# Optimization experiments

Hardware: AMD Instinct MI355X
Metric: run time of the kernel (lower is better)

The kernel has to match this reference:

```python
import jax, jax.numpy as jnp
import numpy as np

B, S, E, H = 2, 2048, 1024, 16
D = E // H  # head_dim = 64


def setup_inputs() -> dict:
    key = jax.random.key(0)
    ks = jax.random.split(key, 4)
    return {
        "hidden_states": jax.random.normal(ks[0], (B, S, E), jnp.float32),
        "qk_weight": jax.random.normal(ks[1], (E, 2 * E), jnp.float32) * 0.02,
        "qk_bias": jnp.zeros((2 * E,), jnp.float32),
        "v_weight": jax.random.normal(ks[2], (E, E), jnp.float32) * 0.02,
        "v_resid_gain": jnp.ones((), jnp.float32),
        "v_skip_gain": jnp.ones((), jnp.float32),
        "proj_weight": jax.random.normal(ks[3], (E, E), jnp.float32) * 0.02,
        "proj_resid_gain": jnp.ones((), jnp.float32),
        "proj_skip_gain": jnp.ones((), jnp.float32),
        "attn_mat_resid_gain": jnp.ones((H,), jnp.float32),
        "attn_mat_skip_gain": jnp.ones((H,), jnp.float32),
        "centre_attn_gain": jnp.ones((H,), jnp.float32),
    }


def reference(hidden_states, qk_weight, qk_bias, v_weight, v_resid_gain,
              v_skip_gain, proj_weight, proj_resid_gain, proj_skip_gain,
              attn_mat_resid_gain, attn_mat_skip_gain, centre_attn_gain):
    b, s, e = hidden_states.shape
    dt = hidden_states.dtype
    eye_e = jnp.eye(e, dtype=dt)

    # qk_attn: MyConv1D (standard linear), split into query/key
    qk = hidden_states @ qk_weight + qk_bias
    q, k = jnp.split(qk, 2, axis=-1)
    # v_attn: skip MyConv1D -> x @ (resid_gain * W + skip_gain * I), no bias
    v = hidden_states @ (v_resid_gain * v_weight + v_skip_gain * eye_e)

    def split_heads(t):  # [b,s,e] -> [b,h,s,d]
        return t.reshape(b, s, H, D).transpose(0, 2, 1, 3)

    q, k, v = split_heads(q), split_heads(k), split_heads(v)

    # scaled causal attention scores
    scores = jnp.einsum('bhqd,bhkd->bhqk', q, k) / jnp.asarray(D, dt) ** 0.5
    causal = jnp.tril(jnp.ones((s, s), bool))
    scores = jnp.where(causal, scores, jnp.finfo(dt).min)
    attn = jax.nn.softmax(scores, axis=-1)

    # shaped attention: gain-mix softmax probs with identity and causal-uniform
    uniform = jnp.tril(jnp.ones((s, s), dt) / jnp.arange(1, s + 1, dtype=dt)[:, None])
    g_r = attn_mat_resid_gain[None, :, None, None]
    g_s = attn_mat_skip_gain[None, :, None, None]
    g_c = centre_attn_gain[None, :, None, None]
    new_attn = g_r * attn + g_s * jnp.eye(s, dtype=dt) - g_c * uniform

    ctx = jnp.einsum('bhqk,bhkd->bhqd', new_attn, v)
    ctx = ctx.transpose(0, 2, 1, 3).reshape(b, s, e)  # merge heads
    # c_proj: skip MyConv1D, no bias
    out = ctx @ (proj_resid_gain * proj_weight + proj_skip_gain * eye_e)
    return out
```

## Files before the change

kernel.cpp:

```cpp
#include <hip/hip_runtime.h>

typedef __bf16 bf16;
typedef __attribute__((ext_vector_type(8))) __bf16 bf16x8;
typedef __attribute__((ext_vector_type(4))) float f32x4;

union U16x8 { uint4 u; bf16 h[8]; };
union Pack4 { uint2 u2; bf16 h[4]; };

#define QSCALE 0.18033688011112042f

__device__ __forceinline__ void async16(const bf16* g, bf16* l) {
    __builtin_amdgcn_global_load_lds((const __attribute__((address_space(1))) void*)g,
                                     (__attribute__((address_space(3))) void*)l, 16, 0, 0);
}

__device__ const int QT_OF[40] = {15,15,15,15,14,14,14,14,13,13,13,13,12,12,12,12,
                                  11,11,11,10,10,10,9,9,9,8,8,8,7,7,6,6,5,5,4,4,3,2,1,0};
__device__ const int CK_OF[40] = {0,1,2,3,0,1,2,3,0,1,2,3,0,1,2,3,
                                  0,1,2,0,1,2,0,1,2,0,1,2,0,1,0,1,0,1,0,1,0,0,0,0};
__device__ const int BASE_OF[16] = {39,38,37,36,34,32,30,28,25,22,19,16,12,8,4,0};

__global__ void conv_f2b(const float* __restrict__ x, bf16* __restrict__ y, int n) {
    int i = (blockIdx.x * 256 + threadIdx.x) * 4;
    if (i >= n) return;
    float4 f = *(const float4*)(x + i);
    y[i + 0] = (bf16)f.x; y[i + 1] = (bf16)f.y;
    y[i + 2] = (bf16)f.z; y[i + 3] = (bf16)f.w;
}

__global__ void transpose_all(const float* __restrict__ qkw, const float* __restrict__ vw,
                              const float* __restrict__ pw, bf16* __restrict__ qkvT,
                              bf16* __restrict__ pwT,
                              const float* __restrict__ vrg, const float* __restrict__ vsg,
                              const float* __restrict__ prg, const float* __restrict__ psg) {
    const int K = 1024;
    int z = blockIdx.z;
    int N = z == 0 ? 2048 : 1024;
    if ((int)blockIdx.x * 32 >= N) return;
    const float* W = z == 0 ? qkw : (z == 1 ? vw : pw);
    bf16* WT = z == 0 ? qkvT : (z == 1 ? qkvT + (size_t)2 * 1024 * 1024 : pwT);
    float g0 = z == 0 ? 1.f : (z == 1 ? vrg[0] : prg[0]);
    float g1 = z == 0 ? 0.f : (z == 1 ? vsg[0] : psg[0]);

    __shared__ float tile[32][33];
    int n0 = blockIdx.x * 32, k0 = blockIdx.y * 32;
    int tx = threadIdx.x & 31, ty = threadIdx.x >> 5;
    #pragma unroll
    for (int r = 0; r < 32; r += 8)
        tile[ty + r][tx] = W[(size_t)(k0 + ty + r) * N + n0 + tx];
    __syncthreads();
    #pragma unroll
    for (int r = 0; r < 32; r += 8) {
        int n = n0 + ty + r, k = k0 + tx;
        float v = g0 * tile[tx][ty + r] + ((n == k) ? g1 : 0.f);
        if (z == 0 && n < 1024) v *= QSCALE;
        WT[(size_t)n * K + k] = (bf16)v;
    }
}

template<int BN>
__global__ __launch_bounds__(256, 2)
void gemm_bt(const bf16* __restrict__ A, const bf16* __restrict__ BT,
             int M, int N, int K, void* __restrict__ Cout, bf16* __restrict__ C2,
             bf16* __restrict__ C2T, int mode, const float* __restrict__ aux) {
    __shared__ __align__(16) bf16 As[128][64];
    __shared__ __align__(16) bf16 Bs[BN][64];
    constexpr int JF = BN / 32;
    int m0 = blockIdx.y * 128, n0 = blockIdx.x * BN;
    int t = threadIdx.x, lane = t & 63, w = t >> 6;
    int wm = (w >> 1) * 64, wn = (w & 1) * (BN / 2);
    int lrow = lane & 15, lkg = lane >> 4;

    f32x4 acc[4][JF] = {};

    int gsw = ((lane & 7) ^ ((lane >> 3) & 7)) * 8;
    const bf16* Ab = A + (size_t)(m0 + w * 8 + (lane >> 3)) * K + gsw;
    const bf16* Bb = BT + (size_t)(n0 + w * 8 + (lane >> 3)) * K + gsw;

    for (int k0 = 0; k0 < K; k0 += 64) {
        #pragma unroll
        for (int p = 0; p < 4; p++)
            async16(Ab + (size_t)(p * 32) * K + k0, &As[p * 32 + w * 8][0]);
        #pragma unroll
        for (int p = 0; p < BN / 32; p++)
            async16(Bb + (size_t)(p * 32) * K + k0, &Bs[p * 32 + w * 8][0]);
        __syncthreads();
        #pragma unroll
        for (int ks = 0; ks < 2; ks++) {
            bf16x8 af[4], bfr[JF];
            int phys = (((4 * ks + lkg) ^ (lrow & 7)) << 3);
            #pragma unroll
            for (int i = 0; i < 4; i++) af[i] = *(const bf16x8*)&As[wm + i * 16 + lrow][phys];
            #pragma unroll
            for (int j = 0; j < JF; j++) bfr[j] = *(const bf16x8*)&Bs[wn + j * 16 + lrow][phys];
            #pragma unroll
            for (int i = 0; i < 4; i++)
                #pragma unroll
                for (int j = 0; j < JF; j++)
                    acc[i][j] = __builtin_amdgcn_mfma_f32_16x16x32_bf16(af[i], bfr[j], acc[i][j], 0, 0, 0);
        }
        __syncthreads();
    }

    int rgrp = (lane >> 4) * 4;
    #pragma unroll
    for (int i = 0; i < 4; i++) {
        #pragma unroll
        for (int j = 0; j < JF; j++) {
            int col = n0 + wn + j * 16 + lrow;
            int row0 = m0 + wm + i * 16 + rgrp;
            if (mode == 0) {
                if (col < 2048) {
                    float bb = aux[col];
                    if (col < 1024) bb *= QSCALE;
                    #pragma unroll
                    for (int reg = 0; reg < 4; reg++)
                        ((bf16*)Cout)[(size_t)(row0 + reg) * 2048 + col] = (bf16)(acc[i][j][reg] + bb);
                } else {
                    int c = col - 2048;
                    Pack4 p4;
                    #pragma unroll
                    for (int reg = 0; reg < 4; reg++) {
                        bf16 hv = (bf16)acc[i][j][reg];
                        C2[(size_t)(row0 + reg) * 1024 + c] = hv;
                        p4.h[reg] = hv;
                    }
                    *(uint2*)&C2T[(size_t)c * 4096 + row0] = p4.u2;
                }
            } else {
                #pragma unroll
                for (int reg = 0; reg < 4; reg++)
                    ((float*)Cout)[(size_t)(row0 + reg) * N + col] = acc[i][j][reg];
            }
        }
    }
}

__global__ __launch_bounds__(256, 3)
void flash_split(const bf16* __restrict__ qk, const bf16* __restrict__ vT,
                 bf16* __restrict__ Opart, float* __restrict__ lbuf,
                 int S, int E, int H) {
    __shared__ __align__(16) bf16 Ks[2][64][64];
    __shared__ __align__(16) bf16 Vt[2][64][64];
    __shared__ __align__(16) bf16 Ps[4][32][72];

    int item = blockIdx.x, bh = blockIdx.y;
    int qt = QT_OF[item], ck = CK_OF[item];
    int b = bh >> 4, h = bh & 15;
    int q0 = qt * 128;
    int ktstart = ck * 8;
    int nloc = min(8, 2 * (qt + 1) - ktstart);
    int t = threadIdx.x, lane = t & 63, w = t >> 6;
    int lrow = lane & 15, lkg = lane >> 4;
    const int ld = 2 * E;

    const bf16* Qg  = qk + (size_t)(b * S + q0) * ld + h * 64;
    const bf16* Kg0 = qk + (size_t)(b * S) * ld + E + h * 64;
    const bf16* Vg0 = vT + (size_t)(h * 64) * 4096 + b * 2048;

    bf16x8 qf[2][2];
    #pragma unroll
    for (int qg = 0; qg < 2; qg++)
        #pragma unroll
        for (int ks = 0; ks < 2; ks++)
            qf[qg][ks] = *(const bf16x8*)&Qg[(size_t)(32 * w + 16 * qg + lrow) * ld + ks * 32 + lkg * 8];

    f32x4 oacc[4][2] = {};
    float lrun[2] = {0.f, 0.f};

    auto stage = [&](int buf, int kt) {
        int k0 = kt * 64;
        int g = (lane & 7) ^ ((lane >> 3) & 7);
        #pragma unroll
        for (int p = 0; p < 2; p++) {
            int row = w * 8 + p * 32 + (lane >> 3);
            async16(Kg0 + (size_t)(k0 + row) * ld + g * 8, &Ks[buf][row][(lane & 7) * 8]);
            async16(Vg0 + (size_t)row * 4096 + k0 + g * 8, &Vt[buf][row][(lane & 7) * 8]);
        }
    };

    stage(0, ktstart);
    for (int kl = 0; kl < nloc; kl++) {
        int buf = kl & 1;
        int k0 = (ktstart + kl) * 64;
        __syncthreads();
        if (kl + 1 < nloc) stage(1 - buf, ktstart + kl + 1);

        bool skip0 = (k0 > q0 + 32 * w + 15);
        bool skip1 = (k0 > q0 + 32 * w + 31);
        if (skip0 && skip1) continue;

        f32x4 sacc[2][4] = {};
        #pragma unroll
        for (int ks = 0; ks < 2; ks++) {
            bf16x8 ak[4];
            int phys = (((4 * ks + lkg) ^ (lrow & 7)) << 3);
            #pragma unroll
            for (int kf = 0; kf < 4; kf++)
                ak[kf] = *(const bf16x8*)&Ks[buf][16 * kf + lrow][phys];
            #pragma unroll
            for (int kf = 0; kf < 4; kf++)
                sacc[0][kf] = __builtin_amdgcn_mfma_f32_16x16x32_bf16(ak[kf], qf[0][ks], sacc[0][kf], 0, 0, 0);
            if (!skip1)
                #pragma unroll
                for (int kf = 0; kf < 4; kf++)
                    sacc[1][kf] = __builtin_amdgcn_mfma_f32_16x16x32_bf16(ak[kf], qf[1][ks], sacc[1][kf], 0, 0, 0);
        }

        #pragma unroll
        for (int qg = 0; qg < 2; qg++) {
            if ((qg == 0 && skip0) || (qg == 1 && skip1)) continue;
            int kmin = q0 + 32 * w + 16 * qg;
            bool diag = (k0 + 63 > kmin);
            int qrow = kmin + lrow;
            float rsum = 0.f;
            #pragma unroll
            for (int kf = 0; kf < 4; kf++) {
                Pack4 p4;
                #pragma unroll
                for (int r = 0; r < 4; r++) {
                    float sv = sacc[qg][kf][r];
                    if (diag && (k0 + 16 * kf + 4 * lkg + r > qrow)) sv = -1e30f;
                    float p = exp2f(sv);
                    rsum += p;
                    p4.h[r] = (bf16)p;
                }
                *(uint2*)&Ps[w][16 * qg + lrow][16 * kf + 4 * lkg] = p4.u2;
            }
            lrun[qg] += rsum;
        }

        #pragma unroll
        for (int ks = 0; ks < 2; ks++) {
            bf16x8 av[4];
            int phys = (((4 * ks + lkg) ^ (lrow & 7)) << 3);
            #pragma unroll
            for (int df = 0; df < 4; df++)
                av[df] = *(const bf16x8*)&Vt[buf][16 * df + lrow][phys];
            #pragma unroll
            for (int qg = 0; qg < 2; qg++) {
                if ((qg == 0 && skip0) || (qg == 1 && skip1)) continue;
                bf16x8 bp = *(const bf16x8*)&Ps[w][16 * qg + lrow][ks * 32 + lkg * 8];
                #pragma unroll
                for (int df = 0; df < 4; df++)
                    oacc[df][qg] = __builtin_amdgcn_mfma_f32_16x16x32_bf16(av[df], bp, oacc[df][qg], 0, 0, 0);
            }
        }
    }

    size_t ibase = (size_t)(bh * 40 + item) * 128;
    #pragma unroll
    for (int qg = 0; qg < 2; qg++) {
        #pragma unroll
        for (int df = 0; df < 4; df++) {
            Pack4 p4;
            #pragma unroll
            for (int r = 0; r < 4; r++) p4.h[r] = (bf16)oacc[df][qg][r];
            *(uint2*)&Ps[w][16 * qg + lrow][16 * df + 4 * lkg] = p4.u2;
        }
        float l = lrun[qg];
        l += __shfl_xor(l, 16, 64);
        l += __shfl_xor(l, 32, 64);
        if (lkg == 0) lbuf[ibase + w * 32 + qg * 16 + lrow] = l;
    }
    int r_l = lane >> 1, half = lane & 1;
    bf16* orow = Opart + (ibase + w * 32 + r_l) * 64 + 32 * half;
    #pragma unroll
    for (int c = 0; c < 4; c++)
        *(uint4*)&orow[8 * c] = *(const uint4*)&Ps[w][r_l][32 * half + 8 * c];
}

__global__ void merge_attn(const bf16* __restrict__ Opart, const float* __restrict__ lbuf,
                           bf16* __restrict__ actx) {
    const int S = 2048, E = 1024;
    int qt = blockIdx.x, bh = blockIdx.y;
    int b = bh >> 4, h = bh & 15;
    int nc = (qt >> 2) + 1, base = BASE_OF[qt];
    int t = threadIdx.x;
    int r = t >> 1, dh = (t & 1) * 32;
    int q0 = qt * 128;

    float L = 0.f;
    for (int c = 0; c < nc; c++)
        L += lbuf[(size_t)(bh * 40 + base + c) * 128 + r];
    float inv = 1.f / L;
    float o[32] = {};
    for (int c = 0; c < nc; c++) {
        const bf16* src = Opart + ((size_t)(bh * 40 + base + c) * 128 + r) * 64 + dh;
        #pragma unroll
        for (int g = 0; g < 4; g++) {
            U16x8 u; u.u = *(const uint4*)&src[g * 8];
            #pragma unroll
            for (int j = 0; j < 8; j++) o[g * 8 + j] += (float)u.h[j];
        }
    }
    bf16* dst = actx + (size_t)(b * S + q0 + r) * E + h * 64 + dh;
    #pragma unroll
    for (int g = 0; g < 4; g++) {
        U16x8 u;
        #pragma unroll
        for (int j = 0; j < 8; j++) u.h[j] = (bf16)(o[g * 8 + j] * inv);
        *(uint4*)&dst[g * 8] = u.u;
    }
}

__global__ void chunk_sum(const bf16* __restrict__ v, float* __restrict__ csum) {
    const int S = 2048, E = 1024;
    int colblk = blockIdx.x & 3, chunk = (blockIdx.x >> 2) & 31, b = blockIdx.x >> 7;
    int col = colblk * 256 + threadIdx.x;
    const bf16* p = v + ((size_t)b * S + chunk * 64) * E + col;
    float s = 0.f;
    #pragma unroll 4
    for (int i = 0; i < 64; i++) s += (float)p[(size_t)i * E];
    csum[((size_t)b * 32 + chunk) * E + col] = s;
}
__global__ void chunk_scan(float* __restrict__ csum) {
    const int E = 1024;
    int b = blockIdx.x >> 2;
    int col = (blockIdx.x & 3) * 256 + threadIdx.x;
    float run = 0.f;
    for (int c = 0; c < 32; c++) {
        size_t idx = ((size_t)b * 32 + c) * E + col;
        float x = csum[idx];
        csum[idx] = run;
        run += x;
    }
}
__global__ void apply_combine(const bf16* __restrict__ v, const bf16* __restrict__ actx,
                              const float* __restrict__ csum,
                              const float* __restrict__ gr, const float* __restrict__ gs,
                              const float* __restrict__ gc, bf16* __restrict__ ctx) {
    const int S = 2048, E = 1024;
    int colblk = blockIdx.x & 3, chunk = (blockIdx.x >> 2) & 31, b = blockIdx.x >> 7;
    int col = colblk * 256 + threadIdx.x;
    int h = col >> 6;
    float grh = gr[h], gsh = gs[h], gch = gc[h];
    float run = csum[((size_t)b * 32 + chunk) * E + col];
    const bf16* vp = v + ((size_t)b * S + chunk * 64) * E + col;
    const bf16* ap = actx + ((size_t)b * S + chunk * 64) * E + col;
    bf16* cp = ctx + ((size_t)b * S + chunk * 64) * E + col;
    for (int i = 0; i < 64; i++) {
        int row = chunk * 64 + i;
        float vv = (float)vp[(size_t)i * E];
        run += vv;
        float pm = run / (float)(row + 1);
        cp[(size_t)i * E] = (bf16)(grh * (float)ap[(size_t)i * E] + gsh * vv - gch * pm);
    }
}

extern "C" void kernel_launch(void* const* d_in, const int* in_sizes, int n_in,
                              void* d_out, int out_size, void* d_ws, size_t ws_size,
                              hipStream_t stream) {
    const float* hs  = (const float*)d_in[0];
    const float* qkw = (const float*)d_in[1];
    const float* qkb = (const float*)d_in[2];
    const float* vw  = (const float*)d_in[3];
    const float* vrg = (const float*)d_in[4];
    const float* vsg = (const float*)d_in[5];
    const float* pw  = (const float*)d_in[6];
    const float* prg = (const float*)d_in[7];
    const float* psg = (const float*)d_in[8];
    const float* amr = (const float*)d_in[9];
    const float* ams = (const float*)d_in[10];
    const float* amc = (const float*)d_in[11];
    float* out = (float*)d_out;

    const int B = 2, S = 2048, E = 1024, H = 16, M = B * S;
    char* ws = (char*)d_ws;
    size_t off = 0;
    auto alloc = [&](size_t bytes) { void* p = ws + off; off += (bytes + 255) & ~255ull; return p; };
    bf16* hsb   = (bf16*)alloc((size_t)M * E * 2);
    bf16* qkvT  = (bf16*)alloc((size_t)3 * E * E * 2);
    bf16* pwT   = (bf16*)alloc((size_t)E * E * 2);
    bf16* qko   = (bf16*)alloc((size_t)M * 2 * E * 2);
    bf16* vo    = (bf16*)alloc((size_t)M * E * 2);
    bf16* vT    = (bf16*)alloc((size_t)E * M * 2);
    bf16* actx  = (bf16*)alloc((size_t)M * E * 2);
    float* csum = (float*)alloc((size_t)B * 32 * E * 4);
    bf16* ctxb  = (bf16*)alloc((size_t)M * E * 2);
    bf16* Opart = (bf16*)alloc((size_t)32 * 40 * 128 * 64 * 2);
    float* lbuf = (float*)alloc((size_t)32 * 40 * 128 * 4);

    conv_f2b<<<M * E / 4 / 256, 256, 0, stream>>>(hs, hsb, M * E);
    transpose_all<<<dim3(64, 32, 3), 256, 0, stream>>>(qkw, vw, pw, qkvT, pwT, vrg, vsg, prg, psg);

    gemm_bt<128><<<dim3(3 * E / 128, M / 128), 256, 0, stream>>>(
        hsb, qkvT, M, 3 * E, E, qko, vo, vT, 0, qkb);

    chunk_sum<<<256, 256, 0, stream>>>(vo, csum);
    chunk_scan<<<8, 256, 0, stream>>>(csum);
    flash_split<<<dim3(40, 32), 256, 0, stream>>>(qko, vT, Opart, lbuf, S, E, H);
    merge_attn<<<dim3(16, 32), 256, 0, stream>>>(Opart, lbuf, actx);
    apply_combine<<<256, 256, 0, stream>>>(vo, actx, csum, amr, ams, amc, ctxb);

    gemm_bt<64><<<dim3(E / 64, M / 128), 256, 0, stream>>>(
        ctxb, pwT, M, E, E, out, nullptr, nullptr, 2, nullptr);
}
```

Measured before the change: 223.7 us.

## Fuse attention merge with shaped-attention combine; stage V transpose through LDS

Merges the split-K attention partials and applies the gain mix with identity and causal-uniform in one kernel. The normalized context goes to shared memory instead of a global actx buffer, which removes one launch and a round trip to global memory. The QKV GEMM epilogue now writes the transposed V through an LDS staging tile, so global stores to vT are coalesced rather than strided 8-byte writes. chunk_scan also loads all 32 values up front. The combine phase uses only 128 of 256 threads, each walking 64 rows serially, which may leave the fused kernel underutilised.

```diff
diff --git a/kernel.cpp b/kernel.cpp
--- a/kernel.cpp
+++ b/kernel.cpp
@@ -63,8 +63,9 @@
 void gemm_bt(const bf16* __restrict__ A, const bf16* __restrict__ BT,
              int M, int N, int K, void* __restrict__ Cout, bf16* __restrict__ C2,
              bf16* __restrict__ C2T, int mode, const float* __restrict__ aux) {
-    __shared__ __align__(16) bf16 As[128][64];
-    __shared__ __align__(16) bf16 Bs[BN][64];
+    __shared__ __align__(16) bf16 smem[128 * 64 + BN * 64];
+    bf16 (*As)[64] = (bf16(*)[64])smem;
+    bf16 (*Bs)[64] = (bf16(*)[64])&smem[128 * 64];
     constexpr int JF = BN / 32;
     int m0 = blockIdx.y * 128, n0 = blockIdx.x * BN;
     int t = threadIdx.x, lane = t & 63, w = t >> 6;
@@ -118,19 +119,44 @@
                         ((bf16*)Cout)[(size_t)(row0 + reg) * 2048 + col] = (bf16)(acc[i][j][reg] + bb);
                 } else {
                     int c = col - 2048;
-                    Pack4 p4;
                     #pragma unroll
-                    for (int reg = 0; reg < 4; reg++) {
-                        bf16 hv = (bf16)acc[i][j][reg];
-                        C2[(size_t)(row0 + reg) * 1024 + c] = hv;
-                        p4.h[reg] = hv;
-                    }
-                    *(uint2*)&C2T[(size_t)c * 4096 + row0] = p4.u2;
+                    for (int reg = 0; reg < 4; reg++)
+                        C2[(size_t)(row0 + reg) * 1024 + c] = (bf16)acc[i][j][reg];
                 }
             } else {
                 #pragma unroll
                 for (int reg = 0; reg < 4; reg++)
                     ((float*)Cout)[(size_t)(row0 + reg) * N + col] = acc[i][j][reg];
+            }
+        }
+    }
+
+    if (mode == 0 && n0 >= 2048) {
+        bf16* Tr = smem;
+        #pragma unroll
+        for (int p = 0; p < 2; p++) {
+            __syncthreads();
+            if ((w & 1) == p) {
+                int rbase = wm + rgrp;
+                #pragma unroll
+                for (int i = 0; i < 4; i++) {
+                    #pragma unroll
+                    for (int j = 0; j < JF; j++) {
+                        int c64 = j * 16 + lrow;
+                        Pack4 p4;
+                        #pragma unroll
+                        for (int reg = 0; reg < 4; reg++) p4.h[reg] = (bf16)acc[i][j][reg];
+                        *(uint2*)&Tr[(size_t)c64 * 132 + rbase + i * 16] = p4.u2;
+                    }
+                }
+            }
+            __syncthreads();
+            int cbase = n0 - 2048 + 64 * p;
+            #pragma unroll
+            for (int it = 0; it < 8; it++) {
+                int u = it * 256 + t;
+                int c = u >> 5, rg4 = (u & 31) * 4;
+                *(uint2*)&C2T[(size_t)(cbase + c) * 4096 + m0 + rg4] = *(const uint2*)&Tr[(size_t)c * 132 + rg4];
             }
         }
     }
@@ -270,37 +296,55 @@
         *(uint4*)&orow[8 * c] = *(const uint4*)&Ps[w][r_l][32 * half + 8 * c];
 }
 
-__global__ void merge_attn(const bf16* __restrict__ Opart, const float* __restrict__ lbuf,
-                           bf16* __restrict__ actx) {
+__global__ void merge_combine(const bf16* __restrict__ Opart, const float* __restrict__ lbuf,
+                              const bf16* __restrict__ v, const float* __restrict__ csum,
+                              const float* __restrict__ gr, const float* __restrict__ gs,
+                              const float* __restrict__ gc, bf16* __restrict__ ctx) {
     const int S = 2048, E = 1024;
     int qt = blockIdx.x, bh = blockIdx.y;
     int b = bh >> 4, h = bh & 15;
     int nc = (qt >> 2) + 1, base = BASE_OF[qt];
+    int q0 = qt * 128;
     int t = threadIdx.x;
-    int r = t >> 1, dh = (t & 1) * 32;
-    int q0 = qt * 128;
-
-    float L = 0.f;
-    for (int c = 0; c < nc; c++)
-        L += lbuf[(size_t)(bh * 40 + base + c) * 128 + r];
-    float inv = 1.f / L;
-    float o[32] = {};
-    for (int c = 0; c < nc; c++) {
-        const bf16* src = Opart + ((size_t)(bh * 40 + base + c) * 128 + r) * 64 + dh;
-        #pragma unroll
-        for (int g = 0; g < 4; g++) {
-            U16x8 u; u.u = *(const uint4*)&src[g * 8];
-            #pragma unroll
-            for (int j = 0; j < 8; j++) o[g * 8 + j] += (float)u.h[j];
-        }
-    }
-    bf16* dst = actx + (size_t)(b * S + q0 + r) * E + h * 64 + dh;
-    #pragma unroll
-    for (int g = 0; g < 4; g++) {
-        U16x8 u;
-        #pragma unroll
-        for (int j = 0; j < 8; j++) u.h[j] = (bf16)(o[g * 8 + j] * inv);
-        *(uint4*)&dst[g * 8] = u.u;
+
+    __shared__ float osm[128][65];
+
+    {
+        int r = t >> 1, dh = (t & 1) * 32;
+        float L = 0.f;
+        for (int c = 0; c < nc; c++)
+            L += lbuf[(size_t)(bh * 40 + base + c) * 128 + r];
+        float inv = 1.f / L;
+        float o[32] = {};
+        for (int c = 0; c < nc; c++) {
+            const bf16* src = Opart + ((size_t)(bh * 40 + base + c) * 128 + r) * 64 + dh;
+            #pragma unroll
+            for (int g = 0; g < 4; g++) {
+                U16x8 u; u.u = *(const uint4*)&src[g * 8];
+                #pragma unroll
+                for (int j = 0; j < 8; j++) o[g * 8 + j] += (float)u.h[j];
+            }
+        }
+        #pragma unroll
+        for (int j = 0; j < 32; j++) osm[r][dh + j] = o[j] * inv;
+    }
+    __syncthreads();
+
+    if (t < 128) {
+        int c = t & 63, ckk = t >> 6;
+        int col = h * 64 + c;
+        float grh = gr[h], gsh = gs[h], gch = gc[h];
+        int chunk = (q0 >> 6) + ckk;
+        float run = csum[((size_t)b * 32 + chunk) * E + col];
+        const bf16* vp = v + ((size_t)b * S + chunk * 64) * E + col;
+        bf16* cp = ctx + ((size_t)b * S + chunk * 64) * E + col;
+        for (int i = 0; i < 64; i++) {
+            int row = chunk * 64 + i;
+            float vv = (float)vp[(size_t)i * E];
+            run += vv;
+            float pm = run / (float)(row + 1);
+            cp[(size_t)i * E] = (bf16)(grh * osm[ckk * 64 + i][c] + gsh * vv - gch * pm);
+        }
     }
 }
 
@@ -318,33 +362,16 @@
     const int E = 1024;
     int b = blockIdx.x >> 2;
     int col = (blockIdx.x & 3) * 256 + threadIdx.x;
+    float x[32];
+    #pragma unroll
+    for (int c = 0; c < 32; c++)
+        x[c] = csum[((size_t)b * 32 + c) * E + col];
     float run = 0.f;
+    #pragma unroll
     for (int c = 0; c < 32; c++) {
-        size_t idx = ((size_t)b * 32 + c) * E + col;
-        float x = csum[idx];
-        csum[idx] = run;
-        run += x;
-    }
-}
-__global__ void apply_combine(const bf16* __restrict__ v, const bf16* __restrict__ actx,
-                              const float* __restrict__ csum,
-                              const float* __restrict__ gr, const float* __restrict__ gs,
-                              const float* __restrict__ gc, bf16* __restrict__ ctx) {
-    const int S = 2048, E = 1024;
-    int colblk = blockIdx.x & 3, chunk = (blockIdx.x >> 2) & 31, b = blockIdx.x >> 7;
-    int col = colblk * 256 + threadIdx.x;
-    int h = col >> 6;
-    float grh = gr[h], gsh = gs[h], gch = gc[h];
-    float run = csum[((size_t)b * 32 + chunk) * E + col];
-    const bf16* vp = v + ((size_t)b * S + chunk * 64) * E + col;
-    const bf16* ap = actx + ((size_t)b * S + chunk * 64) * E + col;
-    bf16* cp = ctx + ((size_t)b * S + chunk * 64) * E + col;
-    for (int i = 0; i < 64; i++) {
-        int row = chunk * 64 + i;
-        float vv = (float)vp[(size_t)i * E];
-        run += vv;
-        float pm = run / (float)(row + 1);
-        cp[(size_t)i * E] = (bf16)(grh * (float)ap[(size_t)i * E] + gsh * vv - gch * pm);
+        float cur = x[c];
+        csum[((size_t)b * 32 + c) * E + col] = run;
+        run += cur;
     }
 }
 
@@ -375,7 +402,6 @@
     bf16* qko   = (bf16*)alloc((size_t)M * 2 * E * 2);
     bf16* vo    = (bf16*)alloc((size_t)M * E * 2);
     bf16* vT    = (bf16*)alloc((size_t)E * M * 2);
-    bf16* actx  = (bf16*)alloc((size_t)M * E * 2);
     float* csum = (float*)alloc((size_t)B * 32 * E * 4);
     bf16* ctxb  = (bf16*)alloc((size_t)M * E * 2);
     bf16* Opart = (bf16*)alloc((size_t)32 * 40 * 128 * 64 * 2);
@@ -390,8 +416,7 @@
     chunk_sum<<<256, 256, 0, stream>>>(vo, csum);
     chunk_scan<<<8, 256, 0, stream>>>(csum);
     flash_split<<<dim3(40, 32), 256, 0, stream>>>(qko, vT, Opart, lbuf, S, E, H);
-    merge_attn<<<dim3(16, 32), 256, 0, stream>>>(Opart, lbuf, actx);
-    apply_combine<<<256, 256, 0, stream>>>(vo, actx, csum, amr, ams, amc, ctxb);
+    merge_combine<<<dim3(16, 32), 256, 0, stream>>>(Opart, lbuf, vo, csum, amr, ams, amc, ctxb);
 
     gemm_bt<64><<<dim3(E / 64, M / 128), 256, 0, stream>>>(
         ctxb, pwT, M, E, E, out, nullptr, nullptr, 2, nullptr);
```

Measured after the change: 226.4 us. Within noise of the previous version (+1.2%).

## Fuse prep kernels, fold V chunk sums into GEMM epilogue, merge combine step

Applied to the files above, without the earlier changes.

Merges the hidden-state conversion and weight transposes into one prep launch. The V chunk column sums are now accumulated from the QKV GEMM accumulators with atomics, which removes the separate chunk_sum and chunk_scan kernels. The attention-partial merge is fused with the shaped-attention combine, and the merged context is kept in shared memory rather than written to a global actx buffer. This cuts launch count and global traffic but adds a memset, atomic contention, a serial prefix loop per column in the merge kernel, and a raised occupancy hint on the GEMM that may spill registers.

```diff
diff --git a/kernel.cpp b/kernel.cpp
--- a/kernel.cpp
+++ b/kernel.cpp
@@ -20,49 +20,53 @@
                                   0,1,2,0,1,2,0,1,2,0,1,2,0,1,0,1,0,1,0,1,0,0,0,0};
 __device__ const int BASE_OF[16] = {39,38,37,36,34,32,30,28,25,22,19,16,12,8,4,0};
 
-__global__ void conv_f2b(const float* __restrict__ x, bf16* __restrict__ y, int n) {
-    int i = (blockIdx.x * 256 + threadIdx.x) * 4;
-    if (i >= n) return;
-    float4 f = *(const float4*)(x + i);
-    y[i + 0] = (bf16)f.x; y[i + 1] = (bf16)f.y;
-    y[i + 2] = (bf16)f.z; y[i + 3] = (bf16)f.w;
-}
-
-__global__ void transpose_all(const float* __restrict__ qkw, const float* __restrict__ vw,
-                              const float* __restrict__ pw, bf16* __restrict__ qkvT,
-                              bf16* __restrict__ pwT,
-                              const float* __restrict__ vrg, const float* __restrict__ vsg,
-                              const float* __restrict__ prg, const float* __restrict__ psg) {
+__global__ void prep(const float* __restrict__ hs, bf16* __restrict__ hsb,
+                     const float* __restrict__ qkw, const float* __restrict__ vw,
+                     const float* __restrict__ pw, bf16* __restrict__ qkvT,
+                     bf16* __restrict__ pwT,
+                     const float* __restrict__ vrg, const float* __restrict__ vsg,
+                     const float* __restrict__ prg, const float* __restrict__ psg) {
     const int K = 1024;
-    int z = blockIdx.z;
+    int bx = blockIdx.x;
+    if (bx < 4096) {
+        int i = (bx * 256 + threadIdx.x) * 4;
+        float4 f = *(const float4*)(hs + i);
+        hsb[i + 0] = (bf16)f.x; hsb[i + 1] = (bf16)f.y;
+        hsb[i + 2] = (bf16)f.z; hsb[i + 3] = (bf16)f.w;
+        return;
+    }
+    int r = bx - 4096;
+    int z = r < 2048 ? 0 : (r < 3072 ? 1 : 2);
+    int q = z == 0 ? r : (z == 1 ? r - 2048 : r - 3072);
+    int ntiles = z == 0 ? 64 : 32;
     int N = z == 0 ? 2048 : 1024;
-    if ((int)blockIdx.x * 32 >= N) return;
     const float* W = z == 0 ? qkw : (z == 1 ? vw : pw);
     bf16* WT = z == 0 ? qkvT : (z == 1 ? qkvT + (size_t)2 * 1024 * 1024 : pwT);
     float g0 = z == 0 ? 1.f : (z == 1 ? vrg[0] : prg[0]);
     float g1 = z == 0 ? 0.f : (z == 1 ? vsg[0] : psg[0]);
 
     __shared__ float tile[32][33];
-    int n0 = blockIdx.x * 32, k0 = blockIdx.y * 32;
+    int n0 = (q % ntiles) * 32, k0 = (q / ntiles) * 32;
     int tx = threadIdx.x & 31, ty = threadIdx.x >> 5;
     #pragma unroll
-    for (int r = 0; r < 32; r += 8)
-        tile[ty + r][tx] = W[(size_t)(k0 + ty + r) * N + n0 + tx];
+    for (int rr = 0; rr < 32; rr += 8)
+        tile[ty + rr][tx] = W[(size_t)(k0 + ty + rr) * N + n0 + tx];
     __syncthreads();
     #pragma unroll
-    for (int r = 0; r < 32; r += 8) {
-        int n = n0 + ty + r, k = k0 + tx;
-        float v = g0 * tile[tx][ty + r] + ((n == k) ? g1 : 0.f);
+    for (int rr = 0; rr < 32; rr += 8) {
+        int n = n0 + ty + rr, k = k0 + tx;
+        float v = g0 * tile[tx][ty + rr] + ((n == k) ? g1 : 0.f);
         if (z == 0 && n < 1024) v *= QSCALE;
         WT[(size_t)n * K + k] = (bf16)v;
     }
 }
 
 template<int BN>
-__global__ __launch_bounds__(256, 2)
+__global__ __launch_bounds__(256, 3)
 void gemm_bt(const bf16* __restrict__ A, const bf16* __restrict__ BT,
              int M, int N, int K, void* __restrict__ Cout, bf16* __restrict__ C2,
-             bf16* __restrict__ C2T, int mode, const float* __restrict__ aux) {
+             bf16* __restrict__ C2T, float* __restrict__ csum,
+             int mode, const float* __restrict__ aux) {
     __shared__ __align__(16) bf16 As[128][64];
     __shared__ __align__(16) bf16 Bs[BN][64];
     constexpr int JF = BN / 32;
@@ -134,6 +138,22 @@
             }
         }
     }
+
+    if (mode == 0 && n0 >= 2048) {
+        int chunk = (m0 + wm) >> 6;
+        #pragma unroll
+        for (int j = 0; j < JF; j++) {
+            float s = 0.f;
+            #pragma unroll
+            for (int i = 0; i < 4; i++)
+                #pragma unroll
+                for (int reg = 0; reg < 4; reg++) s += acc[i][j][reg];
+            s += __shfl_xor(s, 16, 64);
+            s += __shfl_xor(s, 32, 64);
+            if (lkg == 0)
+                atomicAdd(&csum[(size_t)chunk * 1024 + (n0 - 2048 + wn + j * 16 + lrow)], s);
+        }
+    }
 }
 
 __global__ __launch_bounds__(256, 3)
@@ -270,81 +290,57 @@
         *(uint4*)&orow[8 * c] = *(const uint4*)&Ps[w][r_l][32 * half + 8 * c];
 }
 
-__global__ void merge_attn(const bf16* __restrict__ Opart, const float* __restrict__ lbuf,
-                           bf16* __restrict__ actx) {
+__global__ void merge_combine(const bf16* __restrict__ Opart, const float* __restrict__ lbuf,
+                              const bf16* __restrict__ v, const float* __restrict__ csum,
+                              const float* __restrict__ gr, const float* __restrict__ gs,
+                              const float* __restrict__ gc, bf16* __restrict__ ctx) {
     const int S = 2048, E = 1024;
     int qt = blockIdx.x, bh = blockIdx.y;
     int b = bh >> 4, h = bh & 15;
     int nc = (qt >> 2) + 1, base = BASE_OF[qt];
+    int q0 = qt * 128;
     int t = threadIdx.x;
-    int r = t >> 1, dh = (t & 1) * 32;
-    int q0 = qt * 128;
-
-    float L = 0.f;
-    for (int c = 0; c < nc; c++)
-        L += lbuf[(size_t)(bh * 40 + base + c) * 128 + r];
-    float inv = 1.f / L;
-    float o[32] = {};
-    for (int c = 0; c < nc; c++) {
-        const bf16* src = Opart + ((size_t)(bh * 40 + base + c) * 128 + r) * 64 + dh;
-        #pragma unroll
-        for (int g = 0; g < 4; g++) {
-            U16x8 u; u.u = *(const uint4*)&src[g * 8];
-            #pragma unroll
-            for (int j = 0; j < 8; j++) o[g * 8 + j] += (float)u.h[j];
-        }
-    }
-    bf16* dst = actx + (size_t)(b * S + q0 + r) * E + h * 64 + dh;
-    #pragma unroll
-    for (int g = 0; g < 4; g++) {
-        U16x8 u;
-        #pragma unroll
-        for (int j = 0; j < 8; j++) u.h[j] = (bf16)(o[g * 8 + j] * inv);
-        *(uint4*)&dst[g * 8] = u.u;
-    }
-}
-
-__global__ void chunk_sum(const bf16* __restrict__ v, float* __restrict__ csum) {
-    const int S = 2048, E = 1024;
-    int colblk = blockIdx.x & 3, chunk = (blockIdx.x >> 2) & 31, b = blockIdx.x >> 7;
-    int col = colblk * 256 + threadIdx.x;
-    const bf16* p = v + ((size_t)b * S + chunk * 64) * E + col;
-    float s = 0.f;
-    #pragma unroll 4
-    for (int i = 0; i < 64; i++) s += (float)p[(size_t)i * E];
-    csum[((size_t)b * 32 + chunk) * E + col] = s;
-}
-__global__ void chunk_scan(float* __restrict__ csum) {
-    const int E = 1024;
-    int b = blockIdx.x >> 2;
-    int col = (blockIdx.x & 3) * 256 + threadIdx.x;
-    float run = 0.f;
-    for (int c = 0; c < 32; c++) {
-        size_t idx = ((size_t)b * 32 + c) * E + col;
-        float x = csum[idx];
-        csum[idx] = run;
-        run += x;
-    }
-}
-__global__ void apply_combine(const bf16* __restrict__ v, const bf16* __restrict__ actx,
-                              const float* __restrict__ csum,
-                              const float* __restrict__ gr, const float* __restrict__ gs,
-                              const float* __restrict__ gc, bf16* __restrict__ ctx) {
-    const int S = 2048, E = 1024;
-    int colblk = blockIdx.x & 3, chunk = (blockIdx.x >> 2) & 31, b = blockIdx.x >> 7;
-    int col = colblk * 256 + threadIdx.x;
-    int h = col >> 6;
-    float grh = gr[h], gsh = gs[h], gch = gc[h];
-    float run = csum[((size_t)b * 32 + chunk) * E + col];
-    const bf16* vp = v + ((size_t)b * S + chunk * 64) * E + col;
-    const bf16* ap = actx + ((size_t)b * S + chunk * 64) * E + col;
-    bf16* cp = ctx + ((size_t)b * S + chunk * 64) * E + col;
-    for (int i = 0; i < 64; i++) {
-        int row = chunk * 64 + i;
-        float vv = (float)vp[(size_t)i * E];
-        run += vv;
-        float pm = run / (float)(row + 1);
-        cp[(size_t)i * E] = (bf16)(grh * (float)ap[(size_t)i * E] + gsh * vv - gch * pm);
+
+    __shared__ bf16 osm[128][66];
+
+    {
+        int r = t >> 1, dh = (t & 1) * 32;
+        float L = 0.f;
+        for (int c = 0; c < nc; c++)
+            L += lbuf[(size_t)(bh * 40 + base + c) * 128 + r];
+        float inv = 1.f / L;
+        float o[32] = {};
+        for (int c = 0; c < nc; c++) {
+            const bf16* src = Opart + ((size_t)(bh * 40 + base + c) * 128 + r) * 64 + dh;
+            #pragma unroll
+            for (int g = 0; g < 4; g++) {
+                U16x8 u; u.u = *(const uint4*)&src[g * 8];
+                #pragma unroll
+                for (int j = 0; j < 8; j++) o[g * 8 + j] += (float)u.h[j];
+            }
+        }
+        #pragma unroll
+        for (int j = 0; j < 32; j++) osm[r][dh + j] = (bf16)(o[j] * inv);
+    }
+    __syncthreads();
+
+    if (t < 128) {
+        int c = t & 63, ckk = t >> 6;
+        int col = h * 64 + c;
+        float grh = gr[h], gsh = gs[h], gch = gc[h];
+        int chunk = (q0 >> 6) + ckk;
+        float run = 0.f;
+        for (int j = 0; j < chunk; j++)
+            run += csum[((size_t)b * 32 + j) * E + col];
+        const bf16* vp = v + ((size_t)b * S + chunk * 64) * E + col;
+        bf16* cp = ctx + ((size_t)b * S + chunk * 64) * E + col;
+        for (int i = 0; i < 64; i++) {
+            int row = chunk * 64 + i;
+            float vv = (float)vp[(size_t)i * E];
+            run += vv;
+            float pm = run / (float)(row + 1);
+            cp[(size_t)i * E] = (bf16)(grh * (float)osm[ckk * 64 + i][c] + gsh * vv - gch * pm);
+        }
     }
 }
 
@@ -375,24 +371,20 @@
     bf16* qko   = (bf16*)alloc((size_t)M * 2 * E * 2);
     bf16* vo    = (bf16*)alloc((size_t)M * E * 2);
     bf16* vT    = (bf16*)alloc((size_t)E * M * 2);
-    bf16* actx  = (bf16*)alloc((size_t)M * E * 2);
     float* csum = (float*)alloc((size_t)B * 32 * E * 4);
     bf16* ctxb  = (bf16*)alloc((size_t)M * E * 2);
     bf16* Opart = (bf16*)alloc((size_t)32 * 40 * 128 * 64 * 2);
     float* lbuf = (float*)alloc((size_t)32 * 40 * 128 * 4);
 
-    conv_f2b<<<M * E / 4 / 256, 256, 0, stream>>>(hs, hsb, M * E);
-    transpose_all<<<dim3(64, 32, 3), 256, 0, stream>>>(qkw, vw, pw, qkvT, pwT, vrg, vsg, prg, psg);
+    hipMemsetAsync(csum, 0, (size_t)B * 32 * E * 4, stream);
+    prep<<<8192, 256, 0, stream>>>(hs, hsb, qkw, vw, pw, qkvT, pwT, vrg, vsg, prg, psg);
 
     gemm_bt<128><<<dim3(3 * E / 128, M / 128), 256, 0, stream>>>(
-        hsb, qkvT, M, 3 * E, E, qko, vo, vT, 0, qkb);
-
-    chunk_sum<<<256, 256, 0, stream>>>(vo, csum);
-    chunk_scan<<<8, 256, 0, stream>>>(csum);
+        hsb, qkvT, M, 3 * E, E, qko, vo, vT, csum, 0, qkb);
+
     flash_split<<<dim3(40, 32), 256, 0, stream>>>(qko, vT, Opart, lbuf, S, E, H);
-    merge_attn<<<dim3(16, 32), 256, 0, stream>>>(Opart, lbuf, actx);
-    apply_combine<<<256, 256, 0, stream>>>(vo, actx, csum, amr, ams, amc, ctxb);
+    merge_combine<<<dim3(16, 32), 256, 0, stream>>>(Opart, lbuf, vo, csum, amr, ams, amc, ctxb);
 
     gemm_bt<64><<<dim3(E / 64, M / 128), 256, 0, stream>>>(
-        ctxb, pwT, M, E, E, out, nullptr, nullptr, 2, nullptr);
-}
+        ctxb, pwT, M, E, E, out, nullptr, nullptr, nullptr, 2, nullptr);
+}
```

Measured after the change: 216.5 us. 1.03x faster.
